# Optimization experiments

Hardware: AMD Instinct MI355X
Metric: run time of the kernel (lower is better)

The kernel has to match this reference:

```python
import jax, jax.numpy as jnp
import numpy as np

N_HEAD = 16
HEAD_DIM = 64
R_VALUE = 256
EPS_LN = 1e-5


def _orf(x, omega, b):
    # orthogonal random features: sqrt(2/r) * cos(x @ omega.T + b)
    r = b.shape[0]
    return jnp.sqrt(2.0 / r) * jnp.cos(x @ omega.T + b)


def _layernorm(x, gamma, beta):
    m = jnp.mean(x, axis=-1, keepdims=True)
    v = jnp.var(x, axis=-1, keepdims=True)
    return (x - m) / jnp.sqrt(v + EPS_LN) * gamma + beta


def setup_inputs() -> dict:
    key = jax.random.key(0)
    ks = jax.random.split(key, 12)
    B, L = 4, 2048
    dm = N_HEAD * HEAD_DIM  # 1024
    inp = {}
    inp["pre_query"] = jax.random.normal(ks[0], (B, L, dm), jnp.float32)
    inp["pre_key"] = jax.random.normal(ks[1], (B, L, dm), jnp.float32)
    inp["pre_value"] = jax.random.normal(ks[2], (B, L, dm), jnp.float32)
    inp["wq"] = jax.random.normal(ks[3], (dm, dm), jnp.float32) * 0.02
    inp["wk"] = jax.random.normal(ks[4], (dm, dm), jnp.float32) * 0.02
    inp["wv"] = jax.random.normal(ks[5], (dm, dm), jnp.float32) * 0.02
    inp["wo"] = jax.random.normal(ks[6], (dm, dm), jnp.float32) * 0.02
    inp["gamma"] = jnp.ones((dm,), jnp.float32)
    inp["beta"] = jnp.zeros((dm,), jnp.float32)
    G = jax.random.normal(ks[7], (R_VALUE, HEAD_DIM), jnp.float32)
    omega, _ = jnp.linalg.qr(G)  # (r, head_dim), orthonormal columns
    inp["omega"] = omega
    inp["b"] = jax.random.uniform(ks[8], (R_VALUE,), jnp.float32) * 2.0 * jnp.pi
    return inp


def reference(pre_query, pre_key, pre_value, wq, wk, wv, wo, gamma, beta, omega, b):
    B, L, dm = pre_query.shape
    H, D = N_HEAD, dm // N_HEAD
    q = (pre_query @ wq.T).reshape(B, L, H, D)
    k = (pre_key @ wk.T).reshape(B, L, H, D)
    v = (pre_value @ wv.T).reshape(B, L, H, D)

    qp = _orf(q, omega, b)  # (B,L,H,R)
    kp = _orf(k, omega, b)  # (B,L,H,R)

    # causal Performer attention as a linear-attention recurrence:
    # S_t = S_{t-1} + k'_t v_t^T ; z_t = z_{t-1} + k'_t
    # out_t = (q'_t . S_t) / clamp(q'_t . z_t)
    R = b.shape[0]
    S0 = jnp.zeros((B, H, R, D), qp.dtype)
    z0 = jnp.zeros((B, H, R), qp.dtype)

    def step(carry, xs):
        S, z = carry
        q_t, k_t, v_t = xs  # (B,H,R),(B,H,R),(B,H,D)
        S = S + k_t[..., :, None] * v_t[..., None, :]
        z = z + k_t
        num = jnp.einsum('bhr,bhrd->bhd', q_t, S)
        den = jnp.clip(jnp.einsum('bhr,bhr->bh', q_t, z), 1e-6, None)
        return (S, z), num / (den[..., None] + 1e-6)

    xs = (qp.transpose(1, 0, 2, 3), kp.transpose(1, 0, 2, 3), v.transpose(1, 0, 2, 3))
    _, out = jax.lax.scan(step, (S0, z0), xs)  # (L,B,H,D)
    out = out.transpose(1, 0, 2, 3).reshape(B, L, dm)

    pre_result = out @ wo.T
    return _layernorm(pre_result + pre_query, gamma, beta)
```

## Files before the change

kernel.cpp:

```cpp
#include <hip/hip_runtime.h>
#include <hip/hip_bf16.h>


typedef float f4 __attribute__((ext_vector_type(4)));
typedef __attribute__((ext_vector_type(8))) short bf16x8;
typedef __attribute__((ext_vector_type(4))) float f32x4;
typedef unsigned short u16x4 __attribute__((ext_vector_type(4)));
typedef unsigned short u16x8 __attribute__((ext_vector_type(8)));

#define B_  4
#define L_  2048
#define H_  16
#define D_  64
#define DM_ 1024
#define R_  256
#define C_  64
#define NC_ (L_ / C_)
#define M_  (B_ * L_)
#define M2_ (M_ * H_)

static __device__ __forceinline__ unsigned short f2bu(float x) {
    __hip_bfloat16 h = __float2bfloat16(x);
    return *(unsigned short*)&h;
}
static __device__ __forceinline__ float bu2f(unsigned short u) {
    union { unsigned int i; float f; } c; c.i = ((unsigned int)u) << 16; return c.f;
}

typedef __attribute__((address_space(3))) void lds_void_t;
typedef __attribute__((address_space(1))) const void gvoid_t;
static __device__ __forceinline__ void gload16(const void* g, void* l) {
    __builtin_amdgcn_global_load_lds((gvoid_t*)g, (lds_void_t*)l, 16, 0, 0);
}

__launch_bounds__(256)
__global__ void cvt_bf16(const float* __restrict__ in, unsigned short* __restrict__ out, int n4) {
    int i = blockIdx.x * 256 + threadIdx.x;
    if (i < n4) {
        f4 v = *(const f4*)&in[(size_t)i * 4];
        ushort4 o;
        o.x = f2bu(v[0]); o.y = f2bu(v[1]); o.z = f2bu(v[2]); o.w = f2bu(v[3]);
        *(ushort4*)&out[(size_t)i * 4] = o;
    }
}

__launch_bounds__(256)
__global__ void cvt_bf16_x3(const float* __restrict__ i0, const float* __restrict__ i1,
                            const float* __restrict__ i2,
                            unsigned short* __restrict__ o0, unsigned short* __restrict__ o1,
                            unsigned short* __restrict__ o2, int n4) {
    const int z = blockIdx.z;
    const float* in = (z == 0) ? i0 : (z == 1) ? i1 : i2;
    unsigned short* out = (z == 0) ? o0 : (z == 1) ? o1 : o2;
    int i = blockIdx.x * 256 + threadIdx.x;
    if (i < n4) {
        f4 v = *(const f4*)&in[(size_t)i * 4];
        ushort4 o;
        o.x = f2bu(v[0]); o.y = f2bu(v[1]); o.z = f2bu(v[2]); o.w = f2bu(v[3]);
        *(ushort4*)&out[(size_t)i * 4] = o;
    }
}

__launch_bounds__(256)
__global__ void gemm_mfma_b3(const unsigned short* __restrict__ A0, const unsigned short* __restrict__ A1,
                             const unsigned short* __restrict__ A2,
                             const unsigned short* __restrict__ B0, const unsigned short* __restrict__ B1,
                             const unsigned short* __restrict__ B2,
                             unsigned short* __restrict__ C0, unsigned short* __restrict__ C1,
                             unsigned short* __restrict__ C2,
                             int M, int N, int K) {
    __shared__ unsigned short Asl[2][128 * 32];
    __shared__ unsigned short Bsl[2][128 * 32];
    const int z = blockIdx.z;
    const unsigned short* A  = (z == 0) ? A0 : (z == 1) ? A1 : A2;
    const unsigned short* Bw = (z == 0) ? B0 : (z == 1) ? B1 : B2;
    unsigned short*       Cb = (z == 0) ? C0 : (z == 1) ? C1 : C2;
    const int t = threadIdx.x;
    const int lane = t & 63, w = t >> 6;
    const int wr = w >> 1, wc = w & 1;
    const int nwg = gridDim.x * gridDim.y;
    const int bid = blockIdx.y * gridDim.x + blockIdx.x;
    const int cpx = nwg >> 3;
    const int swz = (bid & 7) * cpx + (bid >> 3);
    const int row0 = (swz / gridDim.x) * 128, col0 = (swz % gridDim.x) * 128;
    const int sr0 = t >> 2;
    const int ssw = (((t & 3) ^ ((t >> 3) & 3)) * 8);
    const int lg = lane >> 4, lr = lane & 15;
    const int aslot = (lg ^ ((lr >> 1) & 3)) * 8;

#define STAGE_B3(buf, kkk) do { \
        gload16(&A [(size_t)(row0 + sr0)      * K + (kkk) + ssw], &Asl[buf][t * 8]); \
        gload16(&A [(size_t)(row0 + sr0 + 64) * K + (kkk) + ssw], &Asl[buf][(t + 256) * 8]); \
        gload16(&Bw[(size_t)(col0 + sr0)      * K + (kkk) + ssw], &Bsl[buf][t * 8]); \
        gload16(&Bw[(size_t)(col0 + sr0 + 64) * K + (kkk) + ssw], &Bsl[buf][(t + 256) * 8]); \
    } while (0)

    f32x4 acc[4][4] = {};
    STAGE_B3(0, 0);
    __syncthreads();
    int cur = 0;
    for (int kk = 0; kk < K; kk += 32) {
        if (kk + 32 < K) STAGE_B3(cur ^ 1, kk + 32);
        bf16x8 af[4], bfr[4];
#pragma unroll
        for (int m = 0; m < 4; ++m)
            af[m] = *(const bf16x8*)&Asl[cur][(wr * 64 + m * 16 + lr) * 32 + aslot];
#pragma unroll
        for (int n = 0; n < 4; ++n)
            bfr[n] = *(const bf16x8*)&Bsl[cur][(wc * 64 + n * 16 + lr) * 32 + aslot];
#pragma unroll
        for (int m = 0; m < 4; ++m)
#pragma unroll
            for (int n = 0; n < 4; ++n)
                acc[m][n] = __builtin_amdgcn_mfma_f32_16x16x32_bf16(af[m], bfr[n], acc[m][n], 0, 0, 0);
        __syncthreads();
        cur ^= 1;
    }
#undef STAGE_B3
#pragma unroll
    for (int m = 0; m < 4; ++m)
#pragma unroll
        for (int n = 0; n < 4; ++n)
#pragma unroll
            for (int i = 0; i < 4; ++i) {
                int r  = row0 + wr * 64 + m * 16 + lg * 4 + i;
                int cc = col0 + wc * 64 + n * 16 + lr;
                Cb[(size_t)r * N + cc] = f2bu(acc[m][n][i]);
            }
}

__launch_bounds__(256)
__global__ void gemm_out(const unsigned short* __restrict__ A,
                         const unsigned short* __restrict__ Bw,
                         const float* __restrict__ resid,
                         float* __restrict__ Cf,
                         int M, int N, int K) {
    __shared__ unsigned short Asl[2][64 * 32];
    __shared__ unsigned short Bsl[2][128 * 32];
    const int t = threadIdx.x;
    const int lane = t & 63, w = t >> 6;
    const int nwg = gridDim.x * gridDim.y;
    const int bid = blockIdx.y * gridDim.x + blockIdx.x;
    const int cpx = nwg >> 3;
    const int swz = (bid & 7) * cpx + (bid >> 3);
    const int row0 = (swz / gridDim.x) * 64, col0 = (swz % gridDim.x) * 128;
    const int sr0 = t >> 2;
    const int ssw = (((t & 3) ^ ((t >> 3) & 3)) * 8);
    const int lg = lane >> 4, lr = lane & 15;
    const int aslot = (lg ^ ((lr >> 1) & 3)) * 8;

#define STAGE_O(buf, kkk) do { \
        gload16(&A [(size_t)(row0 + sr0)      * K + (kkk) + ssw], &Asl[buf][t * 8]); \
        gload16(&Bw[(size_t)(col0 + sr0)      * K + (kkk) + ssw], &Bsl[buf][t * 8]); \
        gload16(&Bw[(size_t)(col0 + sr0 + 64) * K + (kkk) + ssw], &Bsl[buf][(t + 256) * 8]); \
    } while (0)

    f32x4 acc[4][2] = {};
    STAGE_O(0, 0);
    __syncthreads();
    int cur = 0;
    for (int kk = 0; kk < K; kk += 32) {
        if (kk + 32 < K) STAGE_O(cur ^ 1, kk + 32);
        bf16x8 af[4], bfr[2];
#pragma unroll
        for (int m = 0; m < 4; ++m)
            af[m] = *(const bf16x8*)&Asl[cur][(m * 16 + lr) * 32 + aslot];
#pragma unroll
        for (int n = 0; n < 2; ++n)
            bfr[n] = *(const bf16x8*)&Bsl[cur][(w * 32 + n * 16 + lr) * 32 + aslot];
#pragma unroll
        for (int m = 0; m < 4; ++m)
#pragma unroll
            for (int n = 0; n < 2; ++n)
                acc[m][n] = __builtin_amdgcn_mfma_f32_16x16x32_bf16(af[m], bfr[n], acc[m][n], 0, 0, 0);
        __syncthreads();
        cur ^= 1;
    }
#undef STAGE_O
#pragma unroll
    for (int m = 0; m < 4; ++m)
#pragma unroll
        for (int n = 0; n < 2; ++n)
#pragma unroll
            for (int i = 0; i < 4; ++i) {
                int r  = row0 + m * 16 + lg * 4 + i;
                int cc = col0 + w * 32 + n * 16 + lr;
                size_t off = (size_t)r * N + cc;
                Cf[off] = acc[m][n][i] + resid[off];
            }
}

#define RS_STRIDE 272
__launch_bounds__(256)
__global__ void feat_mfma_b2(const unsigned short* __restrict__ X0, const unsigned short* __restrict__ X1,
                             const unsigned short* __restrict__ om,
                             const float* __restrict__ bvec,
                             unsigned short* __restrict__ O0, unsigned short* __restrict__ O1) {
    __shared__ unsigned short Xs[2 * 64 * 32];
    __shared__ unsigned short Pool[64 * RS_STRIDE];
    const int z = blockIdx.z;
    const unsigned short* X = z ? X1 : X0;
    unsigned short* out = z ? O1 : O0;
    const int t = threadIdx.x;
    const int lane = t & 63, w = t >> 6;
    const int lg = lane >> 4, lr = lane & 15;
    const int m0 = blockIdx.x * 64;
    const int aslot = (lg ^ ((lr >> 1) & 3)) * 8;

#pragma unroll
    for (int i = 0; i < 2; ++i) {
        int cch = i * 256 + t;
        int ks = cch >> 8, row = (cch >> 2) & 63;
        int sub = ((cch & 3) ^ ((cch >> 3) & 3)) * 8;
        gload16(&X[(size_t)(m0 + row) * 64 + ks * 32 + sub], &Xs[cch * 8]);
    }
#pragma unroll
    for (int i = 0; i < 8; ++i) {
        int cch = i * 256 + t;
        int ks = cch >> 10, r = (cch >> 2) & 255;
        int sub = ((cch & 3) ^ ((cch >> 3) & 3)) * 8;
        gload16(&om[(size_t)r * 64 + ks * 32 + sub], &Pool[cch * 8]);
    }
    __syncthreads();

    f32x4 acc[4][4] = {};
#pragma unroll
    for (int ks = 0; ks < 2; ++ks) {
        bf16x8 af[4], bfr[4];
#pragma unroll
        for (int m = 0; m < 4; ++m)
            af[m] = *(const bf16x8*)&Xs[ks * 2048 + (m * 16 + lr) * 32 + aslot];
#pragma unroll
        for (int n = 0; n < 4; ++n)
            bfr[n] = *(const bf16x8*)&Pool[ks * 8192 + (w * 64 + n * 16 + lr) * 32 + aslot];
#pragma unroll
        for (int m = 0; m < 4; ++m)
#pragma unroll
            for (int n = 0; n < 4; ++n)
                acc[m][n] = __builtin_amdgcn_mfma_f32_16x16x32_bf16(af[m], bfr[n], acc[m][n], 0, 0, 0);
    }
    __syncthreads();

    const float scale = 0.08838834764831845f;
#pragma unroll
    for (int n = 0; n < 4; ++n) {
        const int col = w * 64 + n * 16 + lr;
        const float bb = bvec[col];
#pragma unroll
        for (int m = 0; m < 4; ++m)
#pragma unroll
            for (int ii = 0; ii < 4; ++ii)
                Pool[(m * 16 + lg * 4 + ii) * RS_STRIDE + col] = f2bu(scale * __cosf(acc[m][n][ii] + bb));
    }
    __syncthreads();
#pragma unroll
    for (int i = 0; i < 8; ++i) {
        int cch = i * 256 + t;
        int row = cch >> 5, colc = (cch & 31) * 8;
        u16x8 vv = *(const u16x8*)&Pool[row * RS_STRIDE + colc];
        *(u16x8*)&out[(size_t)(m0 + row) * 256 + colc] = vv;
    }
}

__launch_bounds__(256)
__global__ void passA_mfma(const unsigned short* __restrict__ kp, const unsigned short* __restrict__ vb,
                           unsigned short* __restrict__ kvT, float* __restrict__ ksum) {
    __shared__ __align__(16) unsigned short KPt[256][72];
    __shared__ __align__(16) unsigned short Vt[64][72];
    const int c = blockIdx.x, h = blockIdx.y, bz = blockIdx.z;
    const int t = threadIdx.x;
    const int lane = t & 63, w = t >> 6;
    const int lg = lane >> 4, lr = lane & 15;
    const int l0 = c * C_;
    const int bh = bz * H_ + h;

    {
        const int l4 = (t & 15) * 4, rs = (t >> 4) * 16;
        u16x8 row[4][2];
#pragma unroll
        for (int i = 0; i < 4; ++i) {
            const unsigned short* src = &kp[((size_t)(bz * L_ + l0 + l4 + i) * H_ + h) * R_ + rs];
            row[i][0] = *(const u16x8*)src;
            row[i][1] = *(const u16x8*)(src + 8);
        }
#pragma unroll
        for (int q = 0; q < 16; ++q) {
            u16x4 pk = { row[0][q >> 3][q & 7], row[1][q >> 3][q & 7],
                         row[2][q >> 3][q & 7], row[3][q >> 3][q & 7] };
            *(u16x4*)&KPt[rs + q][l4] = pk;
        }
    }
    {
        const int d4 = (t & 15) * 4, ls = (t >> 4) * 4;
        u16x4 x[4];
#pragma unroll
        for (int i = 0; i < 4; ++i)
            x[i] = *(const u16x4*)&vb[(size_t)(bz * L_ + l0 + ls + i) * DM_ + h * 64 + d4];
#pragma unroll
        for (int q = 0; q < 4; ++q) {
            u16x4 pk = { x[0][q], x[1][q], x[2][q], x[3][q] };
            *(u16x4*)&Vt[d4 + q][ls] = pk;
        }
    }
    __syncthreads();

    f32x4 acc[4][4] = {};
#pragma unroll
    for (int ks = 0; ks < 2; ++ks) {
        bf16x8 af[4], bfr[4];
#pragma unroll
        for (int m = 0; m < 4; ++m)
            af[m] = *(const bf16x8*)&KPt[64 * w + 16 * m + lr][ks * 32 + lg * 8];
#pragma unroll
        for (int n = 0; n < 4; ++n)
            bfr[n] = *(const bf16x8*)&Vt[16 * n + lr][ks * 32 + lg * 8];
#pragma unroll
        for (int m = 0; m < 4; ++m)
#pragma unroll
            for (int n = 0; n < 4; ++n)
                acc[m][n] = __builtin_amdgcn_mfma_f32_16x16x32_bf16(af[m], bfr[n], acc[m][n], 0, 0, 0);
    }
    size_t sbase = ((size_t)(bh * NC_ + c)) * 64 * R_;
#pragma unroll
    for (int n = 0; n < 4; ++n)
#pragma unroll
        for (int m = 0; m < 4; ++m) {
            int d = 16 * n + lr;
            int r = 64 * w + 16 * m + lg * 4;
            u16x4 pk = { f2bu(acc[m][n][0]), f2bu(acc[m][n][1]),
                         f2bu(acc[m][n][2]), f2bu(acc[m][n][3]) };
            *(u16x4*)&kvT[sbase + (size_t)d * R_ + r] = pk;
        }
    {
        float s = 0.f;
#pragma unroll
        for (int j = 0; j < 8; ++j) {
            u16x8 vv = *(const u16x8*)&KPt[t][j * 8];
#pragma unroll
            for (int q = 0; q < 8; ++q) s += bu2f(vv[q]);
        }
        ksum[((size_t)(bh * NC_ + c)) * R_ + t] = s;
    }
}

__launch_bounds__(256)
__global__ void passB_chain(unsigned short* __restrict__ kvT, float* __restrict__ ksum) {
    const int bx = blockIdx.x, h = blockIdx.y, bz = blockIdx.z;
    const int t = threadIdx.x;
    const int bh = bz * H_ + h;
    const int idx = bx * 256 + t;
    const int d = idx >> 6;
    const int rg = (idx & 63) * 4;
    size_t base = ((size_t)bh * NC_ * 64 + d) * R_ + rg;
    const size_t cstride = (size_t)64 * R_;
    float run0 = 0.f, run1 = 0.f, run2 = 0.f, run3 = 0.f;
    for (int c = 0; c < NC_; ++c) {
        size_t ix = base + (size_t)c * cstride;
        u16x4 v = *(const u16x4*)&kvT[ix];
        u16x4 o = { f2bu(run0), f2bu(run1), f2bu(run2), f2bu(run3) };
        *(u16x4*)&kvT[ix] = o;
        run0 += bu2f(v[0]); run1 += bu2f(v[1]);
        run2 += bu2f(v[2]); run3 += bu2f(v[3]);
    }
    if (bx == 0) {
        float rz = 0.f;
        for (int c = 0; c < NC_; ++c) {
            size_t ix = ((size_t)bh * NC_ + c) * R_ + t;
            float tmp = ksum[ix];
            ksum[ix] = rz;
            rz += tmp;
        }
    }
}

__launch_bounds__(256)
__global__ void passC_mfma(const unsigned short* __restrict__ qp, const unsigned short* __restrict__ kp,
                           const unsigned short* __restrict__ vb, const unsigned short* __restrict__ kvT,
                           const float* __restrict__ zpref, unsigned short* __restrict__ attnb) {
    __shared__ __align__(16) unsigned short Sl[64 * 256];
    __shared__ __align__(16) unsigned short Vt[80][72];
    __shared__ __align__(16) unsigned short As[64][72];

    const int c = blockIdx.x, h = blockIdx.y, bz = blockIdx.z;
    const int t = threadIdx.x;
    const int lane = t & 63, w = t >> 6;
    const int lg = lane >> 4, lr = lane & 15;
    const int l0 = c * C_;
    const int bh = bz * H_ + h;
    const size_t sbase = ((size_t)(bh * NC_ + c)) * 64 * R_;
    const size_t zbase = ((size_t)(bh * NC_ + c)) * R_;

#pragma unroll
    for (int i = 0; i < 8; ++i) {
        int idx = i * 256 + t;
        int row = idx >> 5, s = idx & 31;
        gload16(&kvT[sbase + (size_t)row * R_ + ((s ^ (row & 7)) << 3)], &Sl[idx * 8]);
    }

    {
        const int d4 = (t & 15) * 4, ls = (t >> 4) * 4;
        u16x4 x[4];
#pragma unroll
        for (int i = 0; i < 4; ++i)
            x[i] = *(const u16x4*)&vb[(size_t)(bz * L_ + l0 + ls + i) * DM_ + h * 64 + d4];
#pragma unroll
        for (int q = 0; q < 4; ++q) {
            u16x4 pk = { x[0][q], x[1][q], x[2][q], x[3][q] };
            *(u16x4*)&Vt[d4 + q][ls] = pk;
        }
    }
    if (t < 16) {
        u16x4 ones = { 0x3F80, 0x3F80, 0x3F80, 0x3F80 };
        *(u16x4*)&Vt[64][t * 4] = ones;
    }

    const size_t qrow = ((size_t)(bz * L_ + l0 + 16 * w + lr) * H_ + h) * R_;
    bf16x8 aq[8];
#pragma unroll
    for (int ks = 0; ks < 8; ++ks) aq[ks] = *(const bf16x8*)&qp[qrow + ks * 32 + lg * 8];

    f32x4 sacc[4] = {};
#pragma unroll
    for (int half = 0; half < 2; ++half) {
        bf16x8 bk[4][4];
#pragma unroll
        for (int k2 = 0; k2 < 4; ++k2)
#pragma unroll
            for (int n = 0; n < 4; ++n)
                bk[k2][n] = *(const bf16x8*)&kp[((size_t)(bz * L_ + l0 + 16 * n + lr) * H_ + h) * R_
                                                + (half * 4 + k2) * 32 + lg * 8];
        __builtin_amdgcn_s_setprio(1);
#pragma unroll
        for (int k2 = 0; k2 < 4; ++k2)
#pragma unroll
            for (int n = 0; n < 4; ++n)
                sacc[n] = __builtin_amdgcn_mfma_f32_16x16x32_bf16(aq[half * 4 + k2], bk[k2][n], sacc[n], 0, 0, 0);
        __builtin_amdgcn_s_setprio(0);
    }
#pragma unroll
    for (int n = 0; n < 4; ++n)
#pragma unroll
        for (int ii = 0; ii < 4; ++ii) {
            int i_loc = 16 * w + lg * 4 + ii;
            int j_loc = 16 * n + lr;
            As[i_loc][j_loc] = (j_loc <= i_loc) ? f2bu(sacc[n][ii]) : (unsigned short)0;
        }

    u16x8 zu[8];
#pragma unroll
    for (int ks = 0; ks < 8; ++ks) {
        f4 z0 = *(const f4*)&zpref[zbase + ks * 32 + lg * 8];
        f4 z1 = *(const f4*)&zpref[zbase + ks * 32 + lg * 8 + 4];
        zu[ks] = u16x8{ f2bu(z0[0]), f2bu(z0[1]), f2bu(z0[2]), f2bu(z0[3]),
                        f2bu(z1[0]), f2bu(z1[1]), f2bu(z1[2]), f2bu(z1[3]) };
    }
    __syncthreads();

    f32x4 oacc[4] = {};
    f32x4 dacc = {};
    __builtin_amdgcn_s_setprio(1);
#pragma unroll
    for (int ks = 0; ks < 8; ++ks) {
#pragma unroll
        for (int n = 0; n < 4; ++n) {
            int row = 16 * n + lr;
            int slot = (ks * 4 + lg) ^ (lr & 7);
            bf16x8 bs = *(const bf16x8*)&Sl[row * 256 + slot * 8];
            oacc[n] = __builtin_amdgcn_mfma_f32_16x16x32_bf16(aq[ks], bs, oacc[n], 0, 0, 0);
        }
        dacc = __builtin_amdgcn_mfma_f32_16x16x32_bf16(aq[ks], *(bf16x8*)&zu[ks], dacc, 0, 0, 0);
    }

    f32x4 racc = {};
#pragma unroll
    for (int ks = 0; ks < 2; ++ks) {
        bf16x8 aa = *(const bf16x8*)&As[16 * w + lr][ks * 32 + lg * 8];
#pragma unroll
        for (int n = 0; n < 4; ++n) {
            bf16x8 bv = *(const bf16x8*)&Vt[16 * n + lr][ks * 32 + lg * 8];
            oacc[n] = __builtin_amdgcn_mfma_f32_16x16x32_bf16(aa, bv, oacc[n], 0, 0, 0);
        }
        bf16x8 b4 = *(const bf16x8*)&Vt[64 + lr][ks * 32 + lg * 8];
        racc = __builtin_amdgcn_mfma_f32_16x16x32_bf16(aa, b4, racc, 0, 0, 0);
    }
    __builtin_amdgcn_s_setprio(0);

#pragma unroll
    for (int ii = 0; ii < 4; ++ii) {
        float rs_ = __shfl(racc[ii], lane & 48, 64);
        float den = rs_ + dacc[ii];
        float inv = 1.f / (fmaxf(den, 1e-6f) + 1e-6f);
#pragma unroll
        for (int n = 0; n < 4; ++n)
            attnb[(size_t)(bz * L_ + l0 + 16 * w + lg * 4 + ii) * DM_ + h * 64 + 16 * n + lr] =
                f2bu(oacc[n][ii] * inv);
    }
}

__launch_bounds__(256)
__global__ void ln_kernel(float* __restrict__ io, const float* __restrict__ gamma,
                          const float* __restrict__ beta) {
    __shared__ float wsum[4], wsum2[4];
    const int row = blockIdx.x;
    const int t = threadIdx.x;
    f4 x = *(const f4*)&io[(size_t)row * DM_ + t * 4];
    float s  = x[0] + x[1] + x[2] + x[3];
    float s2 = x[0]*x[0] + x[1]*x[1] + x[2]*x[2] + x[3]*x[3];
#pragma unroll
    for (int o = 32; o > 0; o >>= 1) {
        s  += __shfl_down(s, o);
        s2 += __shfl_down(s2, o);
    }
    if ((t & 63) == 0) { wsum[t >> 6] = s; wsum2[t >> 6] = s2; }
    __syncthreads();
    s  = wsum[0]  + wsum[1]  + wsum[2]  + wsum[3];
    s2 = wsum2[0] + wsum2[1] + wsum2[2] + wsum2[3];
    const float m = s * (1.f / DM_);
    const float var = s2 * (1.f / DM_) - m * m;
    const float rstd = rsqrtf(var + 1e-5f);
    f4 g  = *(const f4*)&gamma[t * 4];
    f4 bb = *(const f4*)&beta[t * 4];
    f4 o = (x - m) * rstd * g + bb;
    *(f4*)&io[(size_t)row * DM_ + t * 4] = o;
}

extern "C" void kernel_launch(void* const* d_in, const int* in_sizes, int n_in,
                              void* d_out, int out_size, void* d_ws, size_t ws_size,
                              hipStream_t stream) {
    const float* pre_q = (const float*)d_in[0];
    const float* pre_k = (const float*)d_in[1];
    const float* pre_v = (const float*)d_in[2];
    const float* wq    = (const float*)d_in[3];
    const float* wk    = (const float*)d_in[4];
    const float* wv    = (const float*)d_in[5];
    const float* wo    = (const float*)d_in[6];
    const float* gamma = (const float*)d_in[7];
    const float* beta  = (const float*)d_in[8];
    const float* omega = (const float*)d_in[9];
    const float* bvec  = (const float*)d_in[10];

    const size_t NEED = 226ull << 20;
    if (ws_size < NEED) return;

    char* w = (char*)d_ws;
    unsigned short* qp    = (unsigned short*)(w);
    unsigned short* kp    = (unsigned short*)(w + (64ull << 20));
    unsigned short* kvT   = (unsigned short*)(w + (128ull << 20));
    unsigned short* vb    = (unsigned short*)(w + (192ull << 20));
    unsigned short* attnb = (unsigned short*)(w + (208ull << 20));
    float*          ksum  = (float*)(w + (224ull << 20));
    unsigned short* aq    = (unsigned short*)(w);
    unsigned short* ak    = (unsigned short*)(w + (16ull << 20));
    unsigned short* av    = (unsigned short*)(w + (32ull << 20));
    unsigned short* wq_bf = (unsigned short*)(w + (48ull << 20));
    unsigned short* wk_bf = (unsigned short*)(w + (50ull << 20));
    unsigned short* wv_bf = (unsigned short*)(w + (52ull << 20));
    unsigned short* qx    = (unsigned short*)(w + (128ull << 20));
    unsigned short* kx    = (unsigned short*)(w + (144ull << 20));
    unsigned short* om_bf = (unsigned short*)(w + (208ull << 20));
    unsigned short* wo_bf = (unsigned short*)(w + (64ull << 20));
    float*          outb  = (float*)d_out;

    const int n4_big = M_ * DM_ / 4;
    const int n4_w   = DM_ * DM_ / 4;
    const int n4_om  = R_ * D_ / 4;
    dim3 gg3(DM_ / 128, M_ / 128, 3);
    dim3 ggo(DM_ / 128, M_ / 64);

    cvt_bf16_x3<<<dim3((n4_big + 255) / 256, 1, 3), 256, 0, stream>>>(
        pre_q, pre_k, pre_v, aq, ak, av, n4_big);
    cvt_bf16_x3<<<dim3((n4_w + 255) / 256, 1, 3), 256, 0, stream>>>(
        wq, wk, wv, wq_bf, wk_bf, wv_bf, n4_w);
    cvt_bf16<<<(n4_om + 255) / 256, 256, 0, stream>>>(omega, om_bf, n4_om);

    gemm_mfma_b3<<<gg3, 256, 0, stream>>>(aq, ak, av, wq_bf, wk_bf, wv_bf,
                                          qx, kx, vb, M_, DM_, DM_);
    feat_mfma_b2<<<dim3(M2_ / 64, 1, 2), 256, 0, stream>>>(qx, kx, om_bf, bvec, qp, kp);

    passA_mfma<<<dim3(NC_, H_, B_), 256, 0, stream>>>(kp, vb, kvT, ksum);
    passB_chain<<<dim3(16, H_, B_), 256, 0, stream>>>(kvT, ksum);
    passC_mfma<<<dim3(NC_, H_, B_), 256, 0, stream>>>(qp, kp, vb, kvT, ksum, attnb);

    cvt_bf16<<<(n4_w + 255) / 256, 256, 0, stream>>>(wo, wo_bf, n4_w);
    gemm_out<<<ggo, 256, 0, stream>>>(attnb, wo_bf, pre_q, outb, M_, DM_, DM_);
    ln_kernel<<<M_, 256, 0, stream>>>(outb, gamma, beta);
}
```

Baseline: 306.2 us.

## Triple-buffer GEMM LDS staging with partial vmcnt waits

Both bf16 GEMM kernels (the QKV projection and the output projection) move from double to triple buffering of their LDS tiles. Each iteration now issues loads two k-steps ahead. It waits with s_waitcnt vmcnt so that only the oldest stage must have landed, then uses raw s_barrier calls instead of __syncthreads. This keeps more global-to-LDS traffic in flight so load latency is hidden behind MFMA work, at the cost of 50% more shared memory, which may reduce occupancy. The hand-counted vmcnt values must match the number of loads the compiler actually emits per stage.

```diff
diff --git a/kernel.cpp b/kernel.cpp
--- a/kernel.cpp
+++ b/kernel.cpp
@@ -69,8 +69,8 @@
                              unsigned short* __restrict__ C0, unsigned short* __restrict__ C1,
                              unsigned short* __restrict__ C2,
                              int M, int N, int K) {
-    __shared__ unsigned short Asl[2][128 * 32];
-    __shared__ unsigned short Bsl[2][128 * 32];
+    __shared__ unsigned short Asl[3][128 * 32];
+    __shared__ unsigned short Bsl[3][128 * 32];
     const int z = blockIdx.z;
     const unsigned short* A  = (z == 0) ? A0 : (z == 1) ? A1 : A2;
     const unsigned short* Bw = (z == 0) ? B0 : (z == 1) ? B1 : B2;
@@ -94,29 +94,47 @@
         gload16(&Bw[(size_t)(col0 + sr0)      * K + (kkk) + ssw], &Bsl[buf][t * 8]); \
         gload16(&Bw[(size_t)(col0 + sr0 + 64) * K + (kkk) + ssw], &Bsl[buf][(t + 256) * 8]); \
     } while (0)
+#define COMPUTE_B3(buf) do { \
+        bf16x8 af[4], bfr[4]; \
+        _Pragma("unroll") \
+        for (int m = 0; m < 4; ++m) \
+            af[m] = *(const bf16x8*)&Asl[buf][(wr * 64 + m * 16 + lr) * 32 + aslot]; \
+        _Pragma("unroll") \
+        for (int n = 0; n < 4; ++n) \
+            bfr[n] = *(const bf16x8*)&Bsl[buf][(wc * 64 + n * 16 + lr) * 32 + aslot]; \
+        _Pragma("unroll") \
+        for (int m = 0; m < 4; ++m) \
+            _Pragma("unroll") \
+            for (int n = 0; n < 4; ++n) \
+                acc[m][n] = __builtin_amdgcn_mfma_f32_16x16x32_bf16(af[m], bfr[n], acc[m][n], 0, 0, 0); \
+    } while (0)
 
     f32x4 acc[4][4] = {};
     STAGE_B3(0, 0);
-    __syncthreads();
+    STAGE_B3(1, 32);
     int cur = 0;
-    for (int kk = 0; kk < K; kk += 32) {
-        if (kk + 32 < K) STAGE_B3(cur ^ 1, kk + 32);
-        bf16x8 af[4], bfr[4];
-#pragma unroll
-        for (int m = 0; m < 4; ++m)
-            af[m] = *(const bf16x8*)&Asl[cur][(wr * 64 + m * 16 + lr) * 32 + aslot];
-#pragma unroll
-        for (int n = 0; n < 4; ++n)
-            bfr[n] = *(const bf16x8*)&Bsl[cur][(wc * 64 + n * 16 + lr) * 32 + aslot];
-#pragma unroll
-        for (int m = 0; m < 4; ++m)
-#pragma unroll
-            for (int n = 0; n < 4; ++n)
-                acc[m][n] = __builtin_amdgcn_mfma_f32_16x16x32_bf16(af[m], bfr[n], acc[m][n], 0, 0, 0);
-        __syncthreads();
-        cur ^= 1;
-    }
+    for (int kk = 0; kk + 64 < K; kk += 32) {
+        int nx = cur + 2; if (nx >= 3) nx -= 3;
+        STAGE_B3(nx, kk + 64);
+        asm volatile("s_waitcnt vmcnt(8)" ::: "memory");
+        __builtin_amdgcn_sched_barrier(0);
+        __builtin_amdgcn_s_barrier();
+        COMPUTE_B3(cur);
+        __builtin_amdgcn_s_barrier();
+        cur = (cur == 2) ? 0 : cur + 1;
+    }
+    asm volatile("s_waitcnt vmcnt(4)" ::: "memory");
+    __builtin_amdgcn_sched_barrier(0);
+    __builtin_amdgcn_s_barrier();
+    COMPUTE_B3(cur);
+    __builtin_amdgcn_s_barrier();
+    cur = (cur == 2) ? 0 : cur + 1;
+    asm volatile("s_waitcnt vmcnt(0)" ::: "memory");
+    __builtin_amdgcn_sched_barrier(0);
+    __builtin_amdgcn_s_barrier();
+    COMPUTE_B3(cur);
 #undef STAGE_B3
+#undef COMPUTE_B3
 #pragma unroll
     for (int m = 0; m < 4; ++m)
 #pragma unroll
@@ -135,8 +153,8 @@
                          const float* __restrict__ resid,
                          float* __restrict__ Cf,
                          int M, int N, int K) {
-    __shared__ unsigned short Asl[2][64 * 32];
-    __shared__ unsigned short Bsl[2][128 * 32];
+    __shared__ unsigned short Asl[3][64 * 32];
+    __shared__ unsigned short Bsl[3][128 * 32];
     const int t = threadIdx.x;
     const int lane = t & 63, w = t >> 6;
     const int nwg = gridDim.x * gridDim.y;
@@ -154,29 +172,47 @@
         gload16(&Bw[(size_t)(col0 + sr0)      * K + (kkk) + ssw], &Bsl[buf][t * 8]); \
         gload16(&Bw[(size_t)(col0 + sr0 + 64) * K + (kkk) + ssw], &Bsl[buf][(t + 256) * 8]); \
     } while (0)
+#define COMPUTE_O(buf) do { \
+        bf16x8 af[4], bfr[2]; \
+        _Pragma("unroll") \
+        for (int m = 0; m < 4; ++m) \
+            af[m] = *(const bf16x8*)&Asl[buf][(m * 16 + lr) * 32 + aslot]; \
+        _Pragma("unroll") \
+        for (int n = 0; n < 2; ++n) \
+            bfr[n] = *(const bf16x8*)&Bsl[buf][(w * 32 + n * 16 + lr) * 32 + aslot]; \
+        _Pragma("unroll") \
+        for (int m = 0; m < 4; ++m) \
+            _Pragma("unroll") \
+            for (int n = 0; n < 2; ++n) \
+                acc[m][n] = __builtin_amdgcn_mfma_f32_16x16x32_bf16(af[m], bfr[n], acc[m][n], 0, 0, 0); \
+    } while (0)
 
     f32x4 acc[4][2] = {};
     STAGE_O(0, 0);
-    __syncthreads();
+    STAGE_O(1, 32);
     int cur = 0;
-    for (int kk = 0; kk < K; kk += 32) {
-        if (kk + 32 < K) STAGE_O(cur ^ 1, kk + 32);
-        bf16x8 af[4], bfr[2];
-#pragma unroll
-        for (int m = 0; m < 4; ++m)
-            af[m] = *(const bf16x8*)&Asl[cur][(m * 16 + lr) * 32 + aslot];
-#pragma unroll
-        for (int n = 0; n < 2; ++n)
-            bfr[n] = *(const bf16x8*)&Bsl[cur][(w * 32 + n * 16 + lr) * 32 + aslot];
-#pragma unroll
-        for (int m = 0; m < 4; ++m)
-#pragma unroll
-            for (int n = 0; n < 2; ++n)
-                acc[m][n] = __builtin_amdgcn_mfma_f32_16x16x32_bf16(af[m], bfr[n], acc[m][n], 0, 0, 0);
-        __syncthreads();
-        cur ^= 1;
-    }
+    for (int kk = 0; kk + 64 < K; kk += 32) {
+        int nx = cur + 2; if (nx >= 3) nx -= 3;
+        STAGE_O(nx, kk + 64);
+        asm volatile("s_waitcnt vmcnt(6)" ::: "memory");
+        __builtin_amdgcn_sched_barrier(0);
+        __builtin_amdgcn_s_barrier();
+        COMPUTE_O(cur);
+        __builtin_amdgcn_s_barrier();
+        cur = (cur == 2) ? 0 : cur + 1;
+    }
+    asm volatile("s_waitcnt vmcnt(3)" ::: "memory");
+    __builtin_amdgcn_sched_barrier(0);
+    __builtin_amdgcn_s_barrier();
+    COMPUTE_O(cur);
+    __builtin_amdgcn_s_barrier();
+    cur = (cur == 2) ? 0 : cur + 1;
+    asm volatile("s_waitcnt vmcnt(0)" ::: "memory");
+    __builtin_amdgcn_sched_barrier(0);
+    __builtin_amdgcn_s_barrier();
+    COMPUTE_O(cur);
 #undef STAGE_O
+#undef COMPUTE_O
 #pragma unroll
     for (int m = 0; m < 4; ++m)
 #pragma unroll
```

New measurement: 293.2 us. 1.04x faster.
